# Kernel optimization log

Hardware: AMD Instinct MI355X
Metric: run time of the kernel (lower is better)

Reference implementation:

```python
import jax, jax.numpy as jnp
import numpy as np

H, N, L_LEN = 1024, 64, 8192


def setup_inputs() -> dict:
    key = jax.random.key(0)
    k1, k2 = jax.random.split(key)
    # log_dt ~ U[log(dt_min), log(dt_max)] as in the torch __init__
    log_dt = (jax.random.uniform(k1, (H,), dtype=jnp.float32)
              * (np.float32(np.log(0.1)) - np.float32(np.log(0.001)))
              + np.float32(np.log(0.001)))
    # C is a complex (H, N/2) parameter stored as real view (H, N/2, 2)
    C = jax.random.normal(k2, (H, N // 2, 2), dtype=jnp.float32)
    # S4D-Lin init: A = -0.5 + i*pi*n
    log_A_real = jnp.log(0.5 * jnp.ones((H, N // 2), dtype=jnp.float32))
    A_imag = np.float32(np.pi) * jnp.broadcast_to(
        jnp.arange(N // 2, dtype=jnp.float32), (H, N // 2))
    return {"C": C, "log_dt": log_dt, "log_A_real": log_A_real,
            "A_imag": A_imag, "L": L_LEN}


def reference(C, log_dt, log_A_real, A_imag, L):
    dt = jnp.exp(log_dt)                       # (H,)
    Cc = C[..., 0] + 1j * C[..., 1]            # (H, N/2) complex
    A = -jnp.exp(log_A_real) + 1j * A_imag     # (H, N/2) complex
    dtA = A * dt[:, None]                      # (H, N/2)
    Ceff = Cc * (jnp.exp(dtA) - 1.0) / A       # discretization factor folded into C
    # Vandermonde: exp(dtA * l) for l in [0, L)  -> (H, N/2, L) complex
    K = jnp.exp(dtA[:, :, None] * jnp.arange(L, dtype=jnp.float32))
    return 2.0 * jnp.real(jnp.einsum('hn,hnl->hl', Ceff, K))  # (H, L)
```

## Files before the change

### kernel.cpp

```cpp
#include <hip/hip_runtime.h>
#include <math.h>

#define H_DIM 1024
#define N2    32
#define L_LEN 8192
#define TPB   256

#define KS     136
#define A_ROWS 64
#define B_ROWS 64
#define A_OFF  0
#define B_OFF  (A_ROWS * KS)

typedef __bf16 bf16x8 __attribute__((ext_vector_type(8)));
typedef float  f32x4  __attribute__((ext_vector_type(4)));

union B128 { float4 f4; bf16x8 b8; };

__device__ __forceinline__ unsigned pack_bf(float a, float b) {
    return (__float_as_uint(a) >> 16) | (__float_as_uint(b) & 0xFFFF0000u);
}
__device__ __forceinline__ void split_bf(float x, float* hi, float* lo) {
    float h = __uint_as_float(__float_as_uint(x) & 0xFFFF0000u);
    float r = x - h;
    *hi = h;
    *lo = __uint_as_float(__float_as_uint(r) & 0xFFFF0000u);
}
__device__ __forceinline__ float2 cmulf(float2 a, float2 b) {
    return make_float2(fmaf(a.x, b.x, -(a.y * b.y)),
                       fmaf(a.x, b.y,  (a.y * b.x)));
}
__device__ __forceinline__ float2 amp_cis(float amp, double rev) {
    double fr = rev - floor(rev);
    float r = (float)fr;
    float c = __builtin_amdgcn_cosf(r);
    float s = __builtin_amdgcn_sinf(r);
    return make_float2(amp * c, amp * s);
}

#define PRM_W 13

__global__ __launch_bounds__(TPB, 4) void s4d_mfma2_kernel(
    const float* __restrict__ C,
    const float* __restrict__ log_dt,
    const float* __restrict__ log_A_real,
    const float* __restrict__ A_imag,
    float* __restrict__ out)
{
    __shared__ unsigned short smem[(A_ROWS + B_ROWS) * KS];
    __shared__ float prm[N2 * PRM_W];

    const int h   = blockIdx.x;
    const int by  = blockIdx.y;
    const int tid = threadIdx.x;

    if (tid < N2) {
        const int n   = tid;
        const int idx = h * N2 + n;
        float dt  = expf(log_dt[h]);
        float are = -expf(log_A_real[idx]);
        float aim = A_imag[idx];
        float xr  = are * dt;
        float xi  = aim * dt;
        float ex = expf(xr);
        float s  = sinf(xi);
        float c  = cosf(xi);
        float er = ex * c - 1.0f;
        float ei = ex * s;
        float cr = C[idx * 2 + 0];
        float ci = C[idx * 2 + 1];
        float nr = cr * er - ci * ei;
        float ni = cr * ei + ci * er;
        float inv_den = 1.0f / (are * are + aim * aim);
        float Cr = (nr * are + ni * aim) * inv_den;
        float Ci = (ni * are - nr * aim) * inv_den;

        const double rev1 = (double)xi * 0.15915494309189535;
        float* p = &prm[n * PRM_W];
        float2 z    = amp_cis(__expf(xr), rev1);
        float2 z8   = amp_cis(__expf(8.0f   * xr), 8.0   * rev1);
        float2 w    = amp_cis(__expf(64.0f  * xr), 64.0  * rev1);
        float2 w512 = amp_cis(__expf(512.0f * xr), 512.0 * rev1);
        float  bk   = (float)(4096 * by);
        float2 W0   = amp_cis(__expf(bk * xr), 4096.0 * (double)by * rev1);
        p[0]  = 2.0f * Cr;  p[1]  = 2.0f * Ci;
        p[2]  = z.x;        p[3]  = z.y;
        p[4]  = z8.x;       p[5]  = z8.y;
        p[6]  = w.x;        p[7]  = w.y;
        p[8]  = w512.x;     p[9]  = w512.y;
        p[10] = W0.x;       p[11] = W0.y;
    }
    __syncthreads();

    const int n = tid & 31;
    const int g = tid >> 5;
    const float* p = &prm[n * PRM_W];

    {
        float2 w    = make_float2(p[6], p[7]);
        float2 w512 = make_float2(p[8], p[9]);
        float2 V    = make_float2(p[10], p[11]);
        for (int k = 0; k < g; ++k) V = cmulf(V, w512);
        unsigned short* arow0 = smem + A_OFF + (g * 8) * KS;
#pragma unroll
        for (int r = 0; r < 8; ++r) {
            unsigned* wrow = (unsigned*)(arow0 + r * KS);
            float qrh, qrl, qih, qil;
            split_bf(V.x, &qrh, &qrl);
            split_bf(-V.y, &qih, &qil);
            wrow[n]      = pack_bf(qrh, qih);
            wrow[32 + n] = pack_bf(qrl, qil);
            V = cmulf(V, w);
        }
    }

    {
        float2 z  = make_float2(p[2], p[3]);
        float2 z8 = make_float2(p[4], p[5]);
        float2 u  = make_float2(p[0], p[1]);
        for (int k = 0; k < g; ++k) u = cmulf(u, z8);
        unsigned short* brow0 = smem + B_OFF + (g * 8) * KS;
#pragma unroll
        for (int r = 0; r < 8; ++r) {
            unsigned* wrow = (unsigned*)(brow0 + r * KS);
            float prh, prl, pih, pil;
            split_bf(u.x, &prh, &prl);
            split_bf(u.y, &pih, &pil);
            wrow[n]      = pack_bf(prh, pih);
            wrow[32 + n] = pack_bf(prl, pil);
            u = cmulf(u, z);
        }
    }
    __syncthreads();

    const int lane = tid & 63;
    const int w    = tid >> 6;
    const int m    = lane & 15;
    const int q    = lane >> 4;

    const char* sb = (const char*)smem;
    const int arow = (A_OFF + (w * 16 + m) * KS) * 2;
    B128 ah0, ah1, al0, al1;
    ah0.f4 = *(const float4*)(sb + arow + q * 16);
    ah1.f4 = *(const float4*)(sb + arow + q * 16 + 64);
    al0.f4 = *(const float4*)(sb + arow + 128 + q * 16);
    al1.f4 = *(const float4*)(sb + arow + 128 + q * 16 + 64);

    f32x4 acc[4];
#pragma unroll
    for (int it = 0; it < 4; ++it) acc[it] = (f32x4){0.f, 0.f, 0.f, 0.f};

#pragma unroll
    for (int it = 0; it < 4; ++it) {
        const int brow = (B_OFF + (it * 16 + m) * KS) * 2;
        B128 bh0, bh1, bl0, bl1;
        bh0.f4 = *(const float4*)(sb + brow + q * 16);
        bh1.f4 = *(const float4*)(sb + brow + q * 16 + 64);
        bl0.f4 = *(const float4*)(sb + brow + 128 + q * 16);
        bl1.f4 = *(const float4*)(sb + brow + 128 + q * 16 + 64);
        f32x4 a = acc[it];
        a = __builtin_amdgcn_mfma_f32_16x16x32_bf16(ah0.b8, bh0.b8, a, 0, 0, 0);
        a = __builtin_amdgcn_mfma_f32_16x16x32_bf16(ah1.b8, bh1.b8, a, 0, 0, 0);
        a = __builtin_amdgcn_mfma_f32_16x16x32_bf16(ah0.b8, bl0.b8, a, 0, 0, 0);
        a = __builtin_amdgcn_mfma_f32_16x16x32_bf16(ah1.b8, bl1.b8, a, 0, 0, 0);
        a = __builtin_amdgcn_mfma_f32_16x16x32_bf16(al0.b8, bh0.b8, a, 0, 0, 0);
        a = __builtin_amdgcn_mfma_f32_16x16x32_bf16(al1.b8, bh1.b8, a, 0, 0, 0);
        acc[it] = a;
    }

    float* op = out + (size_t)h * L_LEN + (size_t)by * 4096;
#pragma unroll
    for (int it = 0; it < 4; ++it) {
#pragma unroll
        for (int reg = 0; reg < 4; ++reg) {
            int jj  = w * 16 + q * 4 + reg;
            int col = it * 16 + m;
            op[64 * jj + col] = acc[it][reg];
        }
    }
}

extern "C" void kernel_launch(void* const* d_in, const int* in_sizes, int n_in,
                              void* d_out, int out_size, void* d_ws, size_t ws_size,
                              hipStream_t stream) {
    const float* C          = (const float*)d_in[0];
    const float* log_dt     = (const float*)d_in[1];
    const float* log_A_real = (const float*)d_in[2];
    const float* A_imag     = (const float*)d_in[3];
    float* out              = (float*)d_out;

    dim3 grid(H_DIM, 2);
    dim3 block(TPB);
    hipLaunchKernelGGL(s4d_mfma2_kernel, grid, block, 0, stream,
                       C, log_dt, log_A_real, A_imag, out);
}
```

Baseline: 77.94 us.

## Compute full sequence per block and drop low-precision split of Vandermonde factor

Each block now handles one head across all 8192 outputs (128 A rows × 64 B cols) instead of two blocks per head. The A operand (the w^j powers) is stored as a single truncated bf16 value with no hi/lo split, so four MFMAs per tile are issued instead of six. This removes the duplicated per-head setup, halves the grid, and cuts MFMA work. In exchange, precision on the A factor is lower, since truncated bf16 gives about 8 bits of mantissa, which could break tolerance. The block also does more serial work, and there is less parallelism across blocks.

```diff
diff --git a/kernel.cpp b/kernel.cpp
--- a/kernel.cpp
+++ b/kernel.cpp
@@ -6,11 +6,12 @@
 #define L_LEN 8192
 #define TPB   256
 
-#define KS     136
-#define A_ROWS 64
+#define KSA    72
+#define KSB    136
+#define A_ROWS 128
 #define B_ROWS 64
 #define A_OFF  0
-#define B_OFF  (A_ROWS * KS)
+#define B_OFF  (A_ROWS * KSA)
 
 typedef __bf16 bf16x8 __attribute__((ext_vector_type(8)));
 typedef float  f32x4  __attribute__((ext_vector_type(4)));
@@ -38,20 +39,19 @@
     return make_float2(amp * c, amp * s);
 }
 
-#define PRM_W 13
+#define PRM_W 11
 
-__global__ __launch_bounds__(TPB, 4) void s4d_mfma2_kernel(
+__global__ __launch_bounds__(TPB, 4) void s4d_mfma3_kernel(
     const float* __restrict__ C,
     const float* __restrict__ log_dt,
     const float* __restrict__ log_A_real,
     const float* __restrict__ A_imag,
     float* __restrict__ out)
 {
-    __shared__ unsigned short smem[(A_ROWS + B_ROWS) * KS];
+    __shared__ unsigned short smem[A_ROWS * KSA + B_ROWS * KSB];
     __shared__ float prm[N2 * PRM_W];
 
     const int h   = blockIdx.x;
-    const int by  = blockIdx.y;
     const int tid = threadIdx.x;
 
     if (tid < N2) {
@@ -77,18 +77,15 @@
 
         const double rev1 = (double)xi * 0.15915494309189535;
         float* p = &prm[n * PRM_W];
-        float2 z    = amp_cis(__expf(xr), rev1);
-        float2 z8   = amp_cis(__expf(8.0f   * xr), 8.0   * rev1);
-        float2 w    = amp_cis(__expf(64.0f  * xr), 64.0  * rev1);
-        float2 w512 = amp_cis(__expf(512.0f * xr), 512.0 * rev1);
-        float  bk   = (float)(4096 * by);
-        float2 W0   = amp_cis(__expf(bk * xr), 4096.0 * (double)by * rev1);
-        p[0]  = 2.0f * Cr;  p[1]  = 2.0f * Ci;
-        p[2]  = z.x;        p[3]  = z.y;
-        p[4]  = z8.x;       p[5]  = z8.y;
-        p[6]  = w.x;        p[7]  = w.y;
-        p[8]  = w512.x;     p[9]  = w512.y;
-        p[10] = W0.x;       p[11] = W0.y;
+        float2 z  = amp_cis(__expf(xr),            rev1);
+        float2 z8 = amp_cis(__expf(8.0f * xr),     8.0 * rev1);
+        float2 w  = amp_cis(__expf(64.0f * xr),    64.0 * rev1);
+        float2 zK = amp_cis(__expf(1024.0f * xr),  1024.0 * rev1);
+        p[0] = 2.0f * Cr;  p[1] = 2.0f * Ci;
+        p[2] = z.x;        p[3] = z.y;
+        p[4] = z8.x;       p[5] = z8.y;
+        p[6] = w.x;        p[7] = w.y;
+        p[8] = zK.x;       p[9] = zK.y;
     }
     __syncthreads();
 
@@ -97,19 +94,16 @@
     const float* p = &prm[n * PRM_W];
 
     {
-        float2 w    = make_float2(p[6], p[7]);
-        float2 w512 = make_float2(p[8], p[9]);
-        float2 V    = make_float2(p[10], p[11]);
-        for (int k = 0; k < g; ++k) V = cmulf(V, w512);
-        unsigned short* arow0 = smem + A_OFF + (g * 8) * KS;
+        float2 w  = make_float2(p[6], p[7]);
+        float2 zK = make_float2(p[8], p[9]);
+        float2 V  = make_float2(1.0f, 0.0f);
+        for (int k = 0; k < g; ++k) V = cmulf(V, zK);
+        unsigned short* arow0 = smem + A_OFF + (g * 16) * KSA;
 #pragma unroll
-        for (int r = 0; r < 8; ++r) {
-            unsigned* wrow = (unsigned*)(arow0 + r * KS);
-            float qrh, qrl, qih, qil;
-            split_bf(V.x, &qrh, &qrl);
-            split_bf(-V.y, &qih, &qil);
-            wrow[n]      = pack_bf(qrh, qih);
-            wrow[32 + n] = pack_bf(qrl, qil);
+        for (int r = 0; r < 16; ++r) {
+            unsigned* wrow = (unsigned*)(arow0 + r * KSA);
+            wrow[n] = (__float_as_uint(V.x) >> 16)
+                    | ((__float_as_uint(V.y) ^ 0x80000000u) & 0xFFFF0000u);
             V = cmulf(V, w);
         }
     }
@@ -119,10 +113,10 @@
         float2 z8 = make_float2(p[4], p[5]);
         float2 u  = make_float2(p[0], p[1]);
         for (int k = 0; k < g; ++k) u = cmulf(u, z8);
-        unsigned short* brow0 = smem + B_OFF + (g * 8) * KS;
+        unsigned short* brow0 = smem + B_OFF + (g * 8) * KSB;
 #pragma unroll
         for (int r = 0; r < 8; ++r) {
-            unsigned* wrow = (unsigned*)(brow0 + r * KS);
+            unsigned* wrow = (unsigned*)(brow0 + r * KSB);
             float prh, prl, pih, pil;
             split_bf(u.x, &prh, &prl);
             split_bf(u.y, &pih, &pil);
@@ -139,43 +133,52 @@
     const int q    = lane >> 4;
 
     const char* sb = (const char*)smem;
-    const int arow = (A_OFF + (w * 16 + m) * KS) * 2;
-    B128 ah0, ah1, al0, al1;
-    ah0.f4 = *(const float4*)(sb + arow + q * 16);
-    ah1.f4 = *(const float4*)(sb + arow + q * 16 + 64);
-    al0.f4 = *(const float4*)(sb + arow + 128 + q * 16);
-    al1.f4 = *(const float4*)(sb + arow + 128 + q * 16 + 64);
 
-    f32x4 acc[4];
+    B128 ah[2][2];
 #pragma unroll
-    for (int it = 0; it < 4; ++it) acc[it] = (f32x4){0.f, 0.f, 0.f, 0.f};
+    for (int jt = 0; jt < 2; ++jt) {
+        const int abyte = (A_OFF + (w * 32 + jt * 16 + m) * KSA) * 2;
+        ah[jt][0].f4 = *(const float4*)(sb + abyte + q * 16);
+        ah[jt][1].f4 = *(const float4*)(sb + abyte + 64 + q * 16);
+    }
+
+    f32x4 acc[2][4];
+#pragma unroll
+    for (int jt = 0; jt < 2; ++jt)
+#pragma unroll
+        for (int it = 0; it < 4; ++it)
+            acc[jt][it] = (f32x4){0.f, 0.f, 0.f, 0.f};
 
 #pragma unroll
     for (int it = 0; it < 4; ++it) {
-        const int brow = (B_OFF + (it * 16 + m) * KS) * 2;
+        const int bbyte = (B_OFF + (it * 16 + m) * KSB) * 2;
         B128 bh0, bh1, bl0, bl1;
-        bh0.f4 = *(const float4*)(sb + brow + q * 16);
-        bh1.f4 = *(const float4*)(sb + brow + q * 16 + 64);
-        bl0.f4 = *(const float4*)(sb + brow + 128 + q * 16);
-        bl1.f4 = *(const float4*)(sb + brow + 128 + q * 16 + 64);
-        f32x4 a = acc[it];
-        a = __builtin_amdgcn_mfma_f32_16x16x32_bf16(ah0.b8, bh0.b8, a, 0, 0, 0);
-        a = __builtin_amdgcn_mfma_f32_16x16x32_bf16(ah1.b8, bh1.b8, a, 0, 0, 0);
-        a = __builtin_amdgcn_mfma_f32_16x16x32_bf16(ah0.b8, bl0.b8, a, 0, 0, 0);
-        a = __builtin_amdgcn_mfma_f32_16x16x32_bf16(ah1.b8, bl1.b8, a, 0, 0, 0);
-        a = __builtin_amdgcn_mfma_f32_16x16x32_bf16(al0.b8, bh0.b8, a, 0, 0, 0);
-        a = __builtin_amdgcn_mfma_f32_16x16x32_bf16(al1.b8, bh1.b8, a, 0, 0, 0);
-        acc[it] = a;
+        bh0.f4 = *(const float4*)(sb + bbyte + q * 16);
+        bh1.f4 = *(const float4*)(sb + bbyte + 64 + q * 16);
+        bl0.f4 = *(const float4*)(sb + bbyte + 128 + q * 16);
+        bl1.f4 = *(const float4*)(sb + bbyte + 192 + q * 16);
+#pragma unroll
+        for (int jt = 0; jt < 2; ++jt) {
+            f32x4 a = acc[jt][it];
+            a = __builtin_amdgcn_mfma_f32_16x16x32_bf16(ah[jt][0].b8, bh0.b8, a, 0, 0, 0);
+            a = __builtin_amdgcn_mfma_f32_16x16x32_bf16(ah[jt][1].b8, bh1.b8, a, 0, 0, 0);
+            a = __builtin_amdgcn_mfma_f32_16x16x32_bf16(ah[jt][0].b8, bl0.b8, a, 0, 0, 0);
+            a = __builtin_amdgcn_mfma_f32_16x16x32_bf16(ah[jt][1].b8, bl1.b8, a, 0, 0, 0);
+            acc[jt][it] = a;
+        }
     }
 
-    float* op = out + (size_t)h * L_LEN + (size_t)by * 4096;
+    float* op = out + (size_t)h * L_LEN;
 #pragma unroll
-    for (int it = 0; it < 4; ++it) {
+    for (int jt = 0; jt < 2; ++jt) {
 #pragma unroll
-        for (int reg = 0; reg < 4; ++reg) {
-            int jj  = w * 16 + q * 4 + reg;
-            int col = it * 16 + m;
-            op[64 * jj + col] = acc[it][reg];
+        for (int it = 0; it < 4; ++it) {
+#pragma unroll
+            for (int reg = 0; reg < 4; ++reg) {
+                int jj  = w * 32 + jt * 16 + q * 4 + reg;
+                int col = it * 16 + m;
+                op[64 * jj + col] = acc[jt][it][reg];
+            }
         }
     }
 }
@@ -189,8 +192,8 @@
     const float* A_imag     = (const float*)d_in[3];
     float* out              = (float*)d_out;
 
-    dim3 grid(H_DIM, 2);
+    dim3 grid(H_DIM);
     dim3 block(TPB);
-    hipLaunchKernelGGL(s4d_mfma2_kernel, grid, block, 0, stream,
+    hipLaunchKernelGGL(s4d_mfma3_kernel, grid, block, 0, stream,
                        C, log_dt, log_A_real, A_imag, out);
 }
```

Measured after the change: 75.46 us. -3.2%, faster.
